# Performance work log

Measured on AMD Instinct MI355X. Metric: run time of the kernel, lower is better.

## Reference

```python
import jax, jax.numpy as jnp
import numpy as np
from jax import lax

# TT-conv configuration (matches init_kwargs)
M = (4, 8, 8)        # in_c_modes, prod = 256
O = (4, 8, 8)        # out_c_modes, prod = 256
R = (16, 16, 16, 1)  # ranks with trailing 1 appended as in the module
B, H, W = 8, 64, 64
IN_C = int(np.prod(M))


def setup_inputs() -> dict:
    key = jax.random.key(0)
    ks = jax.random.split(key, 6)
    X = jax.random.normal(ks[0], (B, IN_C, H, W), jnp.float32)
    conv_w = jax.random.normal(ks[1], (R[0], 1, 3, 3), jnp.float32) * 0.3
    conv_b = jax.random.normal(ks[2], (R[0],), jnp.float32) * 0.05
    def xavier(k, shape):
        fan_in, fan_out = shape[1], shape[0]
        std = (2.0 / (fan_in + fan_out)) ** 0.5
        return jax.random.normal(k, shape, jnp.float32) * std
    core1 = xavier(ks[3], (O[0] * R[1], R[0] * M[0]))  # (64, 64)
    core2 = xavier(ks[4], (O[1] * R[2], R[1] * M[1]))  # (128, 128)
    core3 = xavier(ks[5], (O[2] * R[3], R[2] * M[2]))  # (8, 128)
    return {"X": X, "conv_w": conv_w, "conv_b": conv_b,
            "core1": core1, "core2": core2, "core3": core3}


def reference(X, conv_w, conv_b, core1, core2, core3):
    b, in_c, h, w = X.shape
    # core0: depth-agnostic 1->r0 conv applied per input channel
    y = lax.conv_general_dilated(
        X.reshape(-1, 1, h, w), conv_w,
        window_strides=(1, 1), padding=((1, 1), (1, 1)),
        dimension_numbers=("NCHW", "OIHW", "NCHW"))
    y = y + conv_b[None, :, None, None]          # (B*in_c, r0, h, w)
    hh, ww = y.shape[-2:]
    # (B, m1, m2, m3, r0, h, w): in_c factored row-major, m1 most significant
    y = y.reshape(b, M[0], M[1], M[2], R[0], hh, ww)
    # TT cores reshaped (o_i, r_{i+1}, r_i, m_i)
    G1 = core1.reshape(O[0], R[1], R[0], M[0])
    G2 = core2.reshape(O[1], R[2], R[1], M[1])
    G3 = core3.reshape(O[2], R[3], R[2], M[2])
    # Full TT contraction chain collapsed into one einsum; s (=r3) has size 1.
    out = jnp.einsum("bijkrhw,auri,cvuj,dsvk->bacdhw",
                     y, G1, G2, G3, optimize=True)
    # channel order (o1, o2, o3) with o3 fastest, as in the torch module
    return out.reshape(b, O[0] * O[1] * O[2], hh, ww)
```

## Files before the change

### kernel.cpp

```cpp
#include <hip/hip_runtime.h>
#include <hip/hip_bf16.h>
#include <stdint.h>

typedef __attribute__((ext_vector_type(8))) short short8;
typedef __attribute__((ext_vector_type(4))) float f32x4;

#define XP_BYTES   17842176
#define XP_PAD     1024
#define OFF_W9     (XP_BYTES + XP_PAD)
#define W9_BYTES   (8*9*256*32*2)
#define OFF_BIAS   (OFF_W9 + W9_BYTES)

__device__ __forceinline__ short f2bf(float f) {
  __hip_bfloat16 h = __float2bfloat16(f);
  return *reinterpret_cast<short*>(&h);
}

__device__ __forceinline__ void gl_lds16(const void* g, void* l) {
  __builtin_amdgcn_global_load_lds(
      (const __attribute__((address_space(1))) void*)g,
      (__attribute__((address_space(3))) void*)l, 16, 0, 0);
}

__global__ void k_weights(const float* __restrict__ core1,
                          const float* __restrict__ core2,
                          const float* __restrict__ core3,
                          const float* __restrict__ convw,
                          const float* __restrict__ convb,
                          short* __restrict__ W9, float* __restrict__ bias) {
  __shared__ float H2s[1024];
  __shared__ float red[256];
  const int o = blockIdx.x, c = threadIdx.x;
  const int a = o >> 6, c2 = (o >> 3) & 7, d = o & 7;
#pragma unroll
  for (int p = 0; p < 4; ++p) {
    int idx = c + (p << 8);
    int k = idx & 7, j = (idx >> 3) & 7, u = idx >> 6;
    float s = 0.f;
#pragma unroll
    for (int v = 0; v < 16; ++v)
      s += core2[(c2 * 16 + v) * 128 + u * 8 + j] * core3[d * 128 + v * 8 + k];
    H2s[idx] = s;
  }
  __syncthreads();
  const int i = c >> 6, j = (c >> 3) & 7, k = c & 7;
  float Wr[16];
#pragma unroll
  for (int r = 0; r < 16; ++r) Wr[r] = 0.f;
  for (int u = 0; u < 16; ++u) {
    float h = H2s[u * 64 + j * 8 + k];
    const float* c1 = core1 + (a * 16 + u) * 64 + i;
#pragma unroll
    for (int r = 0; r < 16; ++r) Wr[r] += c1[r * 4] * h;
  }
  const int cb = c >> 5, cl = c & 31, g = cl >> 3, pos = cl & 7;
  const int gslot = g ^ (o & 3);
#pragma unroll
  for (int t = 0; t < 9; ++t) {
    float s = 0.f;
#pragma unroll
    for (int r = 0; r < 16; ++r) s += Wr[r] * convw[r * 9 + t];
    W9[((size_t)((cb * 9 + t) * 256 + o)) * 32 + gslot * 8 + pos] = f2bf(s);
  }
  float s = 0.f;
#pragma unroll
  for (int r = 0; r < 16; ++r) s += Wr[r] * convb[r];
  red[c] = s;
  __syncthreads();
  for (int st = 128; st > 0; st >>= 1) {
    if (c < st) red[c] += red[c + st];
    __syncthreads();
  }
  if (c == 0) bias[o] = red[0];
}

__global__ void k_pad(const float* __restrict__ X, short* __restrict__ Xp) {
  const int yp = blockIdx.x, b = blockIdx.y, cb = blockIdx.z;
  const int t = threadIdx.x;
  const int x = t & 63, sub = t >> 6;
  const size_t rowg = ((size_t)((b * 8 + cb) * 66 + yp)) * 264;
  const short8 z = (short8){0, 0, 0, 0, 0, 0, 0, 0};
  if (yp == 0 || yp == 65) {
    *(short8*)(Xp + (rowg + (size_t)(x << 2) + sub) * 8) = z;
    if (x < 2)
      *(short8*)(Xp + (rowg + (size_t)((64 + x) << 2) + sub) * 8) = z;
    return;
  }
  const int y = yp - 1, xp = x + 1;
  const int gslot = sub ^ ((xp >> 1) & 3);
  const float* src = X + ((size_t)(b * 256 + cb * 32 + sub * 8) * 64 + y) * 64 + x;
  short8 v;
#pragma unroll
  for (int k = 0; k < 8; ++k) v[k] = f2bf(src[(size_t)k * 4096]);
  *(short8*)(Xp + (rowg + (size_t)(xp << 2) + gslot) * 8) = v;
  if (x < 2)
    *(short8*)(Xp + (rowg + (size_t)((x * 65) << 2) + sub) * 8) = z;
}

__global__ __launch_bounds__(256, 2) void k_gemm(
    const short* __restrict__ Xp, const short* __restrict__ W9,
    const float* __restrict__ bias, float* __restrict__ out) {
  __shared__ __align__(16) short XL[21504];

  const int tid  = threadIdx.x;
  const int lane = tid & 63;
  const int wv   = tid >> 6;
  const int l15  = lane & 15;
  const int gl   = lane >> 4;
  const int h0    = blockIdx.x << 3;
  const int oBase = blockIdx.y << 5;
  const int b     = blockIdx.z;
  const int r0    = wv << 1;

  f32x4 acc[2][2][4];
#pragma unroll
  for (int rr = 0; rr < 2; ++rr)
#pragma unroll
    for (int io = 0; io < 2; ++io)
#pragma unroll
      for (int ip = 0; ip < 4; ++ip)
        acc[rr][io][ip] = (f32x4){0.f, 0.f, 0.f, 0.f};

  for (int cb = 0; cb < 8; ++cb) {
    __syncthreads();
    const size_t xb = ((size_t)(((b << 3) + cb) * 66 + h0) * 66) << 5;
#pragma unroll 1
    for (int q = wv; q < 42; q += 4)
      gl_lds16(Xp + xb + (q << 9) + (lane << 3), &XL[q << 9]);
    __syncthreads();

#pragma unroll
    for (int dx = 0; dx < 3; ++dx) {
      short8 af[3][2];
#pragma unroll
      for (int dy = 0; dy < 3; ++dy)
#pragma unroll
        for (int io = 0; io < 2; ++io) {
          const int t = dy * 3 + dx;
          const int ol = (io << 4) + l15;
          af[dy][io] = *(const short8*)&W9[
              (((size_t)((cb * 9 + t) * 256 + oBase + ol)) << 5) +
              ((gl ^ (l15 & 3)) << 3)];
        }
      short8 bfr[4][4];
#pragma unroll
      for (int xr = 0; xr < 4; ++xr) {
        const int prow = r0 + xr;
#pragma unroll
        for (int ip = 0; ip < 4; ++ip) {
          const int x = (ip << 4) + l15 + dx;
          bfr[xr][ip] = *(const short8*)&XL[
              (((prow * 66 + x) << 2) + (gl ^ ((x >> 1) & 3))) << 3];
        }
      }
#pragma unroll
      for (int dy = 0; dy < 3; ++dy)
#pragma unroll
        for (int io = 0; io < 2; ++io)
#pragma unroll
          for (int ip = 0; ip < 4; ++ip) {
            acc[0][io][ip] = __builtin_amdgcn_mfma_f32_16x16x32_bf16(
                af[dy][io], bfr[dy][ip], acc[0][io][ip], 0, 0, 0);
            acc[1][io][ip] = __builtin_amdgcn_mfma_f32_16x16x32_bf16(
                af[dy][io], bfr[dy + 1][ip], acc[1][io][ip], 0, 0, 0);
          }
    }
  }

#pragma unroll
  for (int rr = 0; rr < 2; ++rr) {
    const int h = h0 + r0 + rr;
#pragma unroll
    for (int io = 0; io < 2; ++io) {
#pragma unroll
      for (int r = 0; r < 4; ++r) {
        const int oG = oBase + (io << 4) + (gl << 2) + r;
        const float bv = bias[oG];
        float* op = out + (((size_t)((b << 8) + oG)) << 12) + (h << 6);
#pragma unroll
        for (int ip = 0; ip < 4; ++ip)
          op[(ip << 4) + l15] = acc[rr][io][ip][r] + bv;
      }
    }
  }
}

extern "C" void kernel_launch(void* const* d_in, const int* in_sizes, int n_in,
                              void* d_out, int out_size, void* d_ws, size_t ws_size,
                              hipStream_t stream) {
  (void)in_sizes; (void)n_in; (void)out_size; (void)ws_size;
  const float* X     = (const float*)d_in[0];
  const float* convw = (const float*)d_in[1];
  const float* convb = (const float*)d_in[2];
  const float* core1 = (const float*)d_in[3];
  const float* core2 = (const float*)d_in[4];
  const float* core3 = (const float*)d_in[5];
  float* out = (float*)d_out;
  char*  ws  = (char*)d_ws;

  short* Xp   = (short*)ws;
  short* W9   = (short*)(ws + OFF_W9);
  float* bias = (float*)(ws + OFF_BIAS);

  k_weights<<<256, 256, 0, stream>>>(core1, core2, core3, convw, convb, W9, bias);
  k_pad    <<<dim3(66, 8, 8), 256, 0, stream>>>(X, Xp);
  k_gemm   <<<dim3(8, 8, 8), 256, 0, stream>>>(Xp, W9, bias, out);
}
```

Before: 138.8 us.

## Double-buffer LDS input tiles and enlarge GEMM block to sixteen rows

The conv-GEMM kernel now stages the next channel block's padded input into a second LDS buffer while computing on the current one, so one barrier per iteration replaces the previous load-then-wait pattern. Blocks grow to 512 threads covering sixteen output rows, which cuts the halo overhead per tile. All nine tap weight fragments are hoisted and loaded once per channel block. The cost is about 150KB of LDS per block, so only one block fits per CU, which lowers occupancy and relies on the prefetch to hide load latency.

```diff
diff --git a/kernel.cpp b/kernel.cpp
--- a/kernel.cpp
+++ b/kernel.cpp
@@ -97,17 +97,17 @@
     *(short8*)(Xp + (rowg + (size_t)((x * 65) << 2) + sub) * 8) = z;
 }
 
-__global__ __launch_bounds__(256, 2) void k_gemm(
+__global__ __launch_bounds__(512, 1) void k_gemm(
     const short* __restrict__ Xp, const short* __restrict__ W9,
     const float* __restrict__ bias, float* __restrict__ out) {
-  __shared__ __align__(16) short XL[21504];
+  __shared__ __align__(16) short XL[2][38400];
 
   const int tid  = threadIdx.x;
   const int lane = tid & 63;
   const int wv   = tid >> 6;
   const int l15  = lane & 15;
   const int gl   = lane >> 4;
-  const int h0    = blockIdx.x << 3;
+  const int h0    = blockIdx.x << 4;
   const int oBase = blockIdx.y << 5;
   const int b     = blockIdx.z;
   const int r0    = wv << 1;
@@ -121,27 +121,41 @@
       for (int ip = 0; ip < 4; ++ip)
         acc[rr][io][ip] = (f32x4){0.f, 0.f, 0.f, 0.f};
 
+  const size_t xrow = ((size_t)(b << 3) * 66 + h0) * 66;
+  {
+    const size_t xb = (((size_t)((b << 3) + 0) * 66 + h0) * 66) << 5;
+#pragma unroll 1
+    for (int q = wv; q < 75; q += 8)
+      gl_lds16(Xp + xb + (q << 9) + (lane << 3), &XL[0][q << 9]);
+  }
+
   for (int cb = 0; cb < 8; ++cb) {
+    short8 af[9][2];
+#pragma unroll
+    for (int t = 0; t < 9; ++t)
+#pragma unroll
+      for (int io = 0; io < 2; ++io) {
+        const int ol = (io << 4) + l15;
+        af[t][io] = *(const short8*)&W9[
+            (((size_t)((cb * 9 + t) * 256 + oBase + ol)) << 5) +
+            ((gl ^ (l15 & 3)) << 3)];
+      }
+    __builtin_amdgcn_sched_barrier(0);
+
     __syncthreads();
-    const size_t xb = ((size_t)(((b << 3) + cb) * 66 + h0) * 66) << 5;
+
+    if (cb < 7) {
+      const size_t xb = (((size_t)((b << 3) + cb + 1) * 66 + h0) * 66) << 5;
+      short* dst = &XL[(cb + 1) & 1][0];
 #pragma unroll 1
-    for (int q = wv; q < 42; q += 4)
-      gl_lds16(Xp + xb + (q << 9) + (lane << 3), &XL[q << 9]);
-    __syncthreads();
-
+      for (int q = wv; q < 75; q += 8)
+        gl_lds16(Xp + xb + (q << 9) + (lane << 3), dst + (q << 9));
+    }
+    __builtin_amdgcn_sched_barrier(0);
+
+    const short* XLc = &XL[cb & 1][0];
 #pragma unroll
     for (int dx = 0; dx < 3; ++dx) {
-      short8 af[3][2];
-#pragma unroll
-      for (int dy = 0; dy < 3; ++dy)
-#pragma unroll
-        for (int io = 0; io < 2; ++io) {
-          const int t = dy * 3 + dx;
-          const int ol = (io << 4) + l15;
-          af[dy][io] = *(const short8*)&W9[
-              (((size_t)((cb * 9 + t) * 256 + oBase + ol)) << 5) +
-              ((gl ^ (l15 & 3)) << 3)];
-        }
       short8 bfr[4][4];
 #pragma unroll
       for (int xr = 0; xr < 4; ++xr) {
@@ -149,23 +163,26 @@
 #pragma unroll
         for (int ip = 0; ip < 4; ++ip) {
           const int x = (ip << 4) + l15 + dx;
-          bfr[xr][ip] = *(const short8*)&XL[
+          bfr[xr][ip] = *(const short8*)&XLc[
               (((prow * 66 + x) << 2) + (gl ^ ((x >> 1) & 3))) << 3];
         }
       }
 #pragma unroll
-      for (int dy = 0; dy < 3; ++dy)
+      for (int dy = 0; dy < 3; ++dy) {
+        const int t = dy * 3 + dx;
 #pragma unroll
         for (int io = 0; io < 2; ++io)
 #pragma unroll
           for (int ip = 0; ip < 4; ++ip) {
             acc[0][io][ip] = __builtin_amdgcn_mfma_f32_16x16x32_bf16(
-                af[dy][io], bfr[dy][ip], acc[0][io][ip], 0, 0, 0);
+                af[t][io], bfr[dy][ip], acc[0][io][ip], 0, 0, 0);
             acc[1][io][ip] = __builtin_amdgcn_mfma_f32_16x16x32_bf16(
-                af[dy][io], bfr[dy + 1][ip], acc[1][io][ip], 0, 0, 0);
+                af[t][io], bfr[dy + 1][ip], acc[1][io][ip], 0, 0, 0);
           }
+      }
     }
   }
+  (void)xrow;
 
 #pragma unroll
   for (int rr = 0; rr < 2; ++rr) {
@@ -204,5 +221,5 @@
 
   k_weights<<<256, 256, 0, stream>>>(core1, core2, core3, convw, convb, W9, bias);
   k_pad    <<<dim3(66, 8, 8), 256, 0, stream>>>(X, Xp);
-  k_gemm   <<<dim3(8, 8, 8), 256, 0, stream>>>(Xp, W9, bias, out);
-}
+  k_gemm   <<<dim3(4, 8, 8), 512, 0, stream>>>(Xp, W9, bias, out);
+}
```

Result: no change. 137.2 us (-1.2%).

## Fuse prep kernels and double-buffer LDS staging in the conv GEMM

Applied to the files above, without the earlier changes.

Merges the weight-building and padding kernels into one launch, which saves a kernel launch. The GEMM tile changes from 32 output channels by 64 columns to 64 output channels by 32 columns. The GEMM double-buffers the input tile in LDS and prefetches the next channel block, split into halves interleaved with MFMA groups under sched_barriers and raised priority, to hide global-to-LDS latency. This costs more registers for accumulators and a more rigid instruction schedule.

```diff
diff --git a/kernel.cpp b/kernel.cpp
--- a/kernel.cpp
+++ b/kernel.cpp
@@ -22,60 +22,64 @@
       (__attribute__((address_space(3))) void*)l, 16, 0, 0);
 }
 
-__global__ void k_weights(const float* __restrict__ core1,
-                          const float* __restrict__ core2,
-                          const float* __restrict__ core3,
-                          const float* __restrict__ convw,
-                          const float* __restrict__ convb,
-                          short* __restrict__ W9, float* __restrict__ bias) {
-  __shared__ float H2s[1024];
-  __shared__ float red[256];
-  const int o = blockIdx.x, c = threadIdx.x;
-  const int a = o >> 6, c2 = (o >> 3) & 7, d = o & 7;
-#pragma unroll
-  for (int p = 0; p < 4; ++p) {
-    int idx = c + (p << 8);
-    int k = idx & 7, j = (idx >> 3) & 7, u = idx >> 6;
+__global__ void k_prep(const float* __restrict__ X,
+                       const float* __restrict__ core1,
+                       const float* __restrict__ core2,
+                       const float* __restrict__ core3,
+                       const float* __restrict__ convw,
+                       const float* __restrict__ convb,
+                       short* __restrict__ Xp,
+                       short* __restrict__ W9, float* __restrict__ bias) {
+  if (blockIdx.x < 256) {
+    __shared__ float H2s[1024];
+    __shared__ float red[256];
+    const int o = blockIdx.x, c = threadIdx.x;
+    const int a = o >> 6, c2 = (o >> 3) & 7, d = o & 7;
+#pragma unroll
+    for (int p = 0; p < 4; ++p) {
+      int idx = c + (p << 8);
+      int k = idx & 7, j = (idx >> 3) & 7, u = idx >> 6;
+      float s = 0.f;
+#pragma unroll
+      for (int v = 0; v < 16; ++v)
+        s += core2[(c2 * 16 + v) * 128 + u * 8 + j] * core3[d * 128 + v * 8 + k];
+      H2s[idx] = s;
+    }
+    __syncthreads();
+    const int i = c >> 6, j = (c >> 3) & 7, k = c & 7;
+    float Wr[16];
+#pragma unroll
+    for (int r = 0; r < 16; ++r) Wr[r] = 0.f;
+    for (int u = 0; u < 16; ++u) {
+      float h = H2s[u * 64 + j * 8 + k];
+      const float* c1 = core1 + (a * 16 + u) * 64 + i;
+#pragma unroll
+      for (int r = 0; r < 16; ++r) Wr[r] += c1[r * 4] * h;
+    }
+    const int cb = c >> 5, cl = c & 31, g = cl >> 3, pos = cl & 7;
+    const int gslot = g ^ (o & 3);
+#pragma unroll
+    for (int t = 0; t < 9; ++t) {
+      float s = 0.f;
+#pragma unroll
+      for (int r = 0; r < 16; ++r) s += Wr[r] * convw[r * 9 + t];
+      W9[((size_t)((cb * 9 + t) * 256 + o)) * 32 + gslot * 8 + pos] = f2bf(s);
+    }
     float s = 0.f;
 #pragma unroll
-    for (int v = 0; v < 16; ++v)
-      s += core2[(c2 * 16 + v) * 128 + u * 8 + j] * core3[d * 128 + v * 8 + k];
-    H2s[idx] = s;
-  }
-  __syncthreads();
-  const int i = c >> 6, j = (c >> 3) & 7, k = c & 7;
-  float Wr[16];
-#pragma unroll
-  for (int r = 0; r < 16; ++r) Wr[r] = 0.f;
-  for (int u = 0; u < 16; ++u) {
-    float h = H2s[u * 64 + j * 8 + k];
-    const float* c1 = core1 + (a * 16 + u) * 64 + i;
-#pragma unroll
-    for (int r = 0; r < 16; ++r) Wr[r] += c1[r * 4] * h;
-  }
-  const int cb = c >> 5, cl = c & 31, g = cl >> 3, pos = cl & 7;
-  const int gslot = g ^ (o & 3);
-#pragma unroll
-  for (int t = 0; t < 9; ++t) {
-    float s = 0.f;
-#pragma unroll
-    for (int r = 0; r < 16; ++r) s += Wr[r] * convw[r * 9 + t];
-    W9[((size_t)((cb * 9 + t) * 256 + o)) * 32 + gslot * 8 + pos] = f2bf(s);
-  }
-  float s = 0.f;
-#pragma unroll
-  for (int r = 0; r < 16; ++r) s += Wr[r] * convb[r];
-  red[c] = s;
-  __syncthreads();
-  for (int st = 128; st > 0; st >>= 1) {
-    if (c < st) red[c] += red[c + st];
+    for (int r = 0; r < 16; ++r) s += Wr[r] * convb[r];
+    red[c] = s;
     __syncthreads();
-  }
-  if (c == 0) bias[o] = red[0];
-}
-
-__global__ void k_pad(const float* __restrict__ X, short* __restrict__ Xp) {
-  const int yp = blockIdx.x, b = blockIdx.y, cb = blockIdx.z;
+    for (int st = 128; st > 0; st >>= 1) {
+      if (c < st) red[c] += red[c + st];
+      __syncthreads();
+    }
+    if (c == 0) bias[o] = red[0];
+    return;
+  }
+  const int p = blockIdx.x - 256;
+  const int cb = p / 528, rem = p % 528;
+  const int b = rem / 66, yp = rem % 66;
   const int t = threadIdx.x;
   const int x = t & 63, sub = t >> 6;
   const size_t rowg = ((size_t)((b * 8 + cb) * 66 + yp)) * 264;
@@ -100,85 +104,131 @@
 __global__ __launch_bounds__(256, 2) void k_gemm(
     const short* __restrict__ Xp, const short* __restrict__ W9,
     const float* __restrict__ bias, float* __restrict__ out) {
-  __shared__ __align__(16) short XL[21504];
+  __shared__ __align__(16) short XL[2][15360];
 
   const int tid  = threadIdx.x;
   const int lane = tid & 63;
   const int wv   = tid >> 6;
   const int l15  = lane & 15;
   const int gl   = lane >> 4;
-  const int h0    = blockIdx.x << 3;
-  const int oBase = blockIdx.y << 5;
+  const int hb    = blockIdx.x;
+  const int h0p   = hb << 3;
+  const int o4    = blockIdx.y & 3;
+  const int xh    = blockIdx.y >> 2;
+  const int oBase = o4 << 6;
+  const int x0    = xh << 5;
+  const int xlo   = xh ? 18 : 0;
   const int b     = blockIdx.z;
-  const int r0    = wv << 1;
-
-  f32x4 acc[2][2][4];
+
+  int xoff[4][3];
+#pragma unroll
+  for (int j = 0; j < 4; ++j)
+#pragma unroll
+    for (int dx = 0; dx < 3; ++dx) {
+      const int x = x0 + l15 + dx;
+      xoff[j][dx] = ((wv << 1) + j) * 1536 + (x - xlo) * 32 +
+                    ((gl ^ ((x >> 1) & 3)) << 3);
+    }
+  const int laneW = ((gl ^ (l15 & 3)) << 3);
+
+  f32x4 acc[2][4][2];
 #pragma unroll
   for (int rr = 0; rr < 2; ++rr)
 #pragma unroll
-    for (int io = 0; io < 2; ++io)
-#pragma unroll
-      for (int ip = 0; ip < 4; ++ip)
+    for (int io = 0; io < 4; ++io)
+#pragma unroll
+      for (int ip = 0; ip < 2; ++ip)
         acc[rr][io][ip] = (f32x4){0.f, 0.f, 0.f, 0.f};
+
+#define STG(CB, BUF, QLO, QHI)                                               \
+  {                                                                          \
+    _Pragma("unroll 1")                                                      \
+    for (int q = (QLO) + wv; q < (QHI); q += 4) {                            \
+      const int row = q / 3, xc = q % 3;                                     \
+      const size_t gg = (((size_t)((b << 3) + (CB)) * 66 + h0p + row) * 264  \
+                         + (xlo << 2) + (xc << 6) + lane) << 3;              \
+      gl_lds16(Xp + gg, &XL[BUF][q << 9]);                                   \
+    }                                                                        \
+  }
+
+  STG(0, 0, 0, 30);
+
+  short8 af0[3][4], af1[3][4];
+  short8 bfr[2][4];
+
+#define AFLOAD(DST, CB, DX)                                                  \
+  {                                                                          \
+    _Pragma("unroll")                                                        \
+    for (int dy = 0; dy < 3; ++dy)                                           \
+      _Pragma("unroll")                                                      \
+      for (int io = 0; io < 4; ++io)                                         \
+        DST[dy][io] = *(const short8*)&W9[                                   \
+            (size_t)(((CB) * 9 + dy * 3 + (DX)) * 256 + oBase + (io << 4)    \
+                     + l15) * 32 + laneW];                                   \
+  }
+
+#define LOADS(BUF, DX, IP)                                                   \
+  {                                                                          \
+    _Pragma("unroll")                                                        \
+    for (int j = 0; j < 4; ++j)                                              \
+      bfr[BUF][j] = *(const short8*)&XLc[xoff[j][DX] + ((IP) << 9)];         \
+  }
+
+#define MM(AF, RB)                                                           \
+  {                                                                          \
+    __builtin_amdgcn_s_setprio(1);                                           \
+    _Pragma("unroll")                                                        \
+    for (int dy = 0; dy < 3; ++dy)                                           \
+      _Pragma("unroll")                                                      \
+      for (int rr = 0; rr < 2; ++rr)                                         \
+        _Pragma("unroll")                                                    \
+        for (int io = 0; io < 4; ++io)                                       \
+          acc[rr][io][ipc] = __builtin_amdgcn_mfma_f32_16x16x32_bf16(        \
+              AF[dy][io], bfr[RB][rr + dy], acc[rr][io][ipc], 0, 0, 0);      \
+    __builtin_amdgcn_s_setprio(0);                                           \
+  }
 
   for (int cb = 0; cb < 8; ++cb) {
     __syncthreads();
-    const size_t xb = ((size_t)(((b << 3) + cb) * 66 + h0) * 66) << 5;
-#pragma unroll 1
-    for (int q = wv; q < 42; q += 4)
-      gl_lds16(Xp + xb + (q << 9) + (lane << 3), &XL[q << 9]);
-    __syncthreads();
-
-#pragma unroll
-    for (int dx = 0; dx < 3; ++dx) {
-      short8 af[3][2];
-#pragma unroll
-      for (int dy = 0; dy < 3; ++dy)
-#pragma unroll
-        for (int io = 0; io < 2; ++io) {
-          const int t = dy * 3 + dx;
-          const int ol = (io << 4) + l15;
-          af[dy][io] = *(const short8*)&W9[
-              (((size_t)((cb * 9 + t) * 256 + oBase + ol)) << 5) +
-              ((gl ^ (l15 & 3)) << 3)];
-        }
-      short8 bfr[4][4];
-#pragma unroll
-      for (int xr = 0; xr < 4; ++xr) {
-        const int prow = r0 + xr;
-#pragma unroll
-        for (int ip = 0; ip < 4; ++ip) {
-          const int x = (ip << 4) + l15 + dx;
-          bfr[xr][ip] = *(const short8*)&XL[
-              (((prow * 66 + x) << 2) + (gl ^ ((x >> 1) & 3))) << 3];
-        }
-      }
-#pragma unroll
-      for (int dy = 0; dy < 3; ++dy)
-#pragma unroll
-        for (int io = 0; io < 2; ++io)
-#pragma unroll
-          for (int ip = 0; ip < 4; ++ip) {
-            acc[0][io][ip] = __builtin_amdgcn_mfma_f32_16x16x32_bf16(
-                af[dy][io], bfr[dy][ip], acc[0][io][ip], 0, 0, 0);
-            acc[1][io][ip] = __builtin_amdgcn_mfma_f32_16x16x32_bf16(
-                af[dy][io], bfr[dy + 1][ip], acc[1][io][ip], 0, 0, 0);
-          }
-    }
-  }
+    const short* XLc = &XL[cb & 1][0];
+
+    AFLOAD(af0, cb, 0);
+    __builtin_amdgcn_sched_barrier(0);
+    if (cb < 7) STG(cb + 1, (cb + 1) & 1, 0, 15);
+    __builtin_amdgcn_sched_barrier(0);
+
+    LOADS(0, 0, 0);
+    { const int ipc = 0; LOADS(1, 0, 1); __builtin_amdgcn_sched_barrier(0); MM(af0, 0); }
+    { const int ipc = 1; LOADS(0, 1, 0); __builtin_amdgcn_sched_barrier(0); MM(af0, 1); }
+
+    AFLOAD(af1, cb, 1);
+    AFLOAD(af0, cb, 2);
+    __builtin_amdgcn_sched_barrier(0);
+    if (cb < 7) STG(cb + 1, (cb + 1) & 1, 15, 30);
+    __builtin_amdgcn_sched_barrier(0);
+
+    { const int ipc = 0; LOADS(1, 1, 1); __builtin_amdgcn_sched_barrier(0); MM(af1, 0); }
+    { const int ipc = 1; LOADS(0, 2, 0); __builtin_amdgcn_sched_barrier(0); MM(af1, 1); }
+    { const int ipc = 0; LOADS(1, 2, 1); __builtin_amdgcn_sched_barrier(0); MM(af0, 0); }
+    { const int ipc = 1;                 __builtin_amdgcn_sched_barrier(0); MM(af0, 1); }
+  }
+#undef MM
+#undef LOADS
+#undef AFLOAD
+#undef STG
 
 #pragma unroll
   for (int rr = 0; rr < 2; ++rr) {
-    const int h = h0 + r0 + rr;
-#pragma unroll
-    for (int io = 0; io < 2; ++io) {
+    const int h = (hb << 3) + (wv << 1) + rr;
+#pragma unroll
+    for (int io = 0; io < 4; ++io) {
 #pragma unroll
       for (int r = 0; r < 4; ++r) {
         const int oG = oBase + (io << 4) + (gl << 2) + r;
         const float bv = bias[oG];
-        float* op = out + (((size_t)((b << 8) + oG)) << 12) + (h << 6);
-#pragma unroll
-        for (int ip = 0; ip < 4; ++ip)
+        float* op = out + (((size_t)((b << 8) + oG)) << 12) + (h << 6) + x0;
+#pragma unroll
+        for (int ip = 0; ip < 2; ++ip)
           op[(ip << 4) + l15] = acc[rr][io][ip][r] + bv;
       }
     }
@@ -202,7 +252,7 @@
   short* W9   = (short*)(ws + OFF_W9);
   float* bias = (float*)(ws + OFF_BIAS);
 
-  k_weights<<<256, 256, 0, stream>>>(core1, core2, core3, convw, convb, W9, bias);
-  k_pad    <<<dim3(66, 8, 8), 256, 0, stream>>>(X, Xp);
-  k_gemm   <<<dim3(8, 8, 8), 256, 0, stream>>>(Xp, W9, bias, out);
-}
+  k_prep<<<4480, 256, 0, stream>>>(X, core1, core2, core3, convw, convb,
+                                   Xp, W9, bias);
+  k_gemm<<<dim3(8, 8, 8), 256, 0, stream>>>(Xp, W9, bias, out);
+}
```

Measured after the change: 136.8 us. No clear change (-1.4%).
